# Kernel optimization log

Measured on AMD Instinct MI355X. Metric: run time of the kernel, lower is better.

Reference implementation:

```python
import jax, jax.numpy as jnp
import numpy as np

B, S, D, H, DFF, NL, VOCAB, SRC = 16, 128, 768, 12, 3072, 6, 32000, 256


def _pe_table():
    pos = np.arange(S)[:, None].astype(np.float32)
    div = np.exp(np.arange(0, D, 2).astype(np.float32) * (-np.log(10000.0) / D))
    pe = np.zeros((S, D), np.float32)
    pe[:, 0::2] = np.sin(pos * div)
    pe[:, 1::2] = np.cos(pos * div)
    return jnp.asarray(pe)


def _ln(x, a, b, eps=1e-6):
    m = jnp.mean(x, axis=-1, keepdims=True)
    v = jnp.mean((x - m) ** 2, axis=-1, keepdims=True)
    return a * (x - m) / jnp.sqrt(v + eps) + b


def _mha(q_in, k_in, v_in, mask, Wq, bq, Wk, bk, Wv, bv, Wo, bo):
    Bq, Sq, Dm = q_in.shape
    Sk = k_in.shape[1]
    dk = Dm // H
    q = (q_in @ Wq + bq).reshape(Bq, Sq, H, dk).transpose(0, 2, 1, 3)
    k = (k_in @ Wk + bk).reshape(Bq, Sk, H, dk).transpose(0, 2, 1, 3)
    v = (v_in @ Wv + bv).reshape(Bq, Sk, H, dk).transpose(0, 2, 1, 3)
    s = jnp.einsum('bhqd,bhkd->bhqk', q, k) / jnp.sqrt(jnp.float32(dk))
    if mask is not None:
        s = jnp.where(mask == 0, jnp.float32(-1e9), s)
    a = jax.nn.softmax(s, axis=-1)
    o = jnp.einsum('bhqk,bhkd->bhqd', a, v).transpose(0, 2, 1, 3).reshape(Bq, Sq, Dm)
    return o @ Wo + bo


def _combined_mask(trg):
    # Vectorized, faithful replica of create_combined_mask (incl. its cumulative
    # cross-batch zeroing: for j in 0..B-2, if padding_start[j]!=0 zero rows
    # >= padding_start[j] of ALL batches b >= j).
    b, s = trg.shape
    is_pad = (trg == 0)
    haspad = jnp.any(is_pad, axis=1)
    start = jnp.where(haspad, jnp.argmax(is_pad, axis=1), 0)  # first pad idx, 0 if none
    c = jnp.where(start == 0, s + 1, start)                   # sentinel = never cut
    cmin = jax.lax.cummin(c)
    r = cmin[jnp.minimum(jnp.arange(b), b - 2)]               # effective cutoff per batch
    look = jnp.tril(jnp.ones((s, s), jnp.float32))
    keep = (jnp.arange(s)[None, :] < r[:, None]).astype(jnp.float32)  # (B,S) rows kept
    return (look[None] * keep[:, :, None])[:, None]           # (B,1,S,S)


def setup_inputs():
    key = jax.random.key(0)
    ks = jax.random.split(key, 16)
    tok = jax.random.randint(ks[0], (B, S), 1, VOCAB)
    lens = jax.random.randint(ks[1], (B,), S // 2, S + 1)
    trg = jnp.where(jnp.arange(S)[None, :] < lens[:, None], tok, 0).astype(jnp.int32)
    e_outputs = jax.random.normal(ks[2], (B, SRC, D), dtype=jnp.float32)
    src_mask = jax.random.randint(ks[3], (B, 1, 1, SRC), 0, 2).at[..., 0].set(1).astype(jnp.int32)
    w = lambda k, shape: (jax.random.normal(k, shape) * 0.02).astype(jnp.float32)
    emb = (jax.random.normal(ks[4], (VOCAB, D)) * 0.1).astype(jnp.float32).at[0].set(0.0)
    return {
        'trg': trg, 'e_outputs': e_outputs, 'src_mask': src_mask,
        'emb': emb,
        'y_param': jax.random.normal(ks[5], (S, D), dtype=jnp.float32),
        'pe_alpha': jnp.float32(1.0),
        'Wq': w(ks[6], (NL, 3, D, D)), 'Wk': w(ks[7], (NL, 3, D, D)),
        'Wv': w(ks[8], (NL, 3, D, D)), 'Wo': w(ks[9], (NL, 3, D, D)),
        'bq': jnp.zeros((NL, 3, D)), 'bk': jnp.zeros((NL, 3, D)),
        'bv': jnp.zeros((NL, 3, D)), 'bo': jnp.zeros((NL, 3, D)),
        'W1': w(ks[10], (NL, D, DFF)), 'b1': jnp.zeros((NL, DFF)),
        'W2': w(ks[11], (NL, DFF, D)), 'b2': jnp.zeros((NL, D)),
        'ln_a': jnp.ones((NL, 5, D)), 'ln_b': jnp.zeros((NL, 5, D)),
        'final_a': jnp.ones((D,)), 'final_b': jnp.zeros((D,)),
    }


def reference(trg, e_outputs, src_mask, emb, y_param, pe_alpha, Wq, Wk, Wv, Wo,
              bq, bk, bv, bo, W1, b1, W2, b2, ln_a, ln_b, final_a, final_b):
    x = emb[trg] + pe_alpha * _pe_table()            # embedding + scaled PE
    y = jnp.broadcast_to(y_param, (trg.shape[0],) + y_param.shape)
    trg_mask = _combined_mask(trg)
    for i in range(Wq.shape[0]):
        x2 = _ln(x, ln_a[i, 0], ln_b[i, 0])
        x = x + _mha(x2, x2, x2, trg_mask, Wq[i, 0], bq[i, 0], Wk[i, 0], bk[i, 0], Wv[i, 0], bv[i, 0], Wo[i, 0], bo[i, 0])
        y2 = _ln(y, ln_a[i, 1], ln_b[i, 1])
        y = y + _mha(y2, e_outputs, e_outputs, src_mask, Wq[i, 1], bq[i, 1], Wk[i, 1], bk[i, 1], Wv[i, 1], bv[i, 1], Wo[i, 1], bo[i, 1])
        x2 = _ln(x, ln_a[i, 2], ln_b[i, 2])
        y3 = _ln(y, ln_a[i, 3], ln_b[i, 3])
        x = x + _mha(x2, y3, y3, None, Wq[i, 2], bq[i, 2], Wk[i, 2], bk[i, 2], Wv[i, 2], bv[i, 2], Wo[i, 2], bo[i, 2])
        x2 = _ln(x, ln_a[i, 4], ln_b[i, 4])
        x = x + jnp.maximum(x2 @ W1[i] + b1[i], 0.0) @ W2[i] + b2[i]
    return _ln(x, final_a, final_b)
```

## Files before the change

kernel.cpp:

```cpp
#include <hip/hip_runtime.h>
#include <math.h>

#define BB 16
#define SS 128
#define DD 768
#define HH 12
#define DKK 64
#define DFFF 3072
#define NLL 6
#define SRCC 256

typedef short bf16x8 __attribute__((ext_vector_type(8)));
typedef float f32x4 __attribute__((ext_vector_type(4)));
typedef unsigned short us8 __attribute__((ext_vector_type(8)));
typedef unsigned short us4 __attribute__((ext_vector_type(4)));

__device__ __forceinline__ unsigned short f2bf(float f) {
  unsigned int u = __builtin_bit_cast(unsigned int, f);
  u = (u + 0x7fff + ((u >> 16) & 1)) >> 16;
  return (unsigned short)u;
}

#define GLOADLDS16(gp, lp)                                              \
  __builtin_amdgcn_global_load_lds(                                     \
      (const __attribute__((address_space(1))) void*)(gp),              \
      (__attribute__((address_space(3))) void*)(lp), 16, 0, 0)

__global__ void embjoint_k(const int* __restrict__ trg, const float* __restrict__ emb,
                           const float* __restrict__ alpha,
                           const float* __restrict__ yp,
                           float* __restrict__ x, float* __restrict__ y) {
  int idx = blockIdx.x * blockDim.x + threadIdx.x;
  int c = idx % (DD / 4);
  int r = idx / (DD / 4);
  if (r >= BB * SS) return;
  int s = r % SS;
  if (blockIdx.y == 0) {
    float al = alpha[0];
    float4 e = *(const float4*)(emb + (size_t)trg[r] * DD + c * 4);
    float coef = -logf(10000.0f) / (float)DD;
    float div0 = expf((float)(4 * c) * coef);
    float div1 = expf((float)(4 * c + 2) * coef);
    float s0, c0, s1, c1;
    sincosf((float)s * div0, &s0, &c0);
    sincosf((float)s * div1, &s1, &c1);
    float4 o;
    o.x = e.x + al * s0; o.y = e.y + al * c0;
    o.z = e.z + al * s1; o.w = e.w + al * c1;
    *(float4*)(x + (size_t)r * DD + c * 4) = o;
  } else {
    *(float4*)(y + (size_t)r * DD + c * 4) = *(const float4*)(yp + (size_t)s * DD + c * 4);
  }
}

__global__ void mb_k(const int* __restrict__ trg, int* __restrict__ rbuf,
                     const float* __restrict__ bq, const float* __restrict__ bk,
                     const float* __restrict__ bv, float* __restrict__ bqkv1,
                     float* __restrict__ bkv2, float* __restrict__ bqkv3) {
  int t = threadIdx.x;
  if (blockIdx.x == 0) {
    __shared__ int first[BB];
    if (t < BB) first[t] = 0x7fffffff;
    __syncthreads();
    int b = t >> 4, p0 = (t & 15) * 8;
    int loc = 0x7fffffff;
#pragma unroll
    for (int i = 0; i < 8; i++) {
      if (trg[b * SS + p0 + i] == 0) { loc = p0 + i; break; }
    }
    atomicMin(&first[b], loc);
    __syncthreads();
    if (t == 0) {
      int cmin = 0x7fffffff;
      int cm[BB];
      for (int bb = 0; bb < BB; bb++) {
        int start = (first[bb] == 0x7fffffff) ? 0 : first[bb];
        int c = (start == 0) ? (SS + 1) : start;
        cmin = min(cmin, c);
        cm[bb] = cmin;
      }
      for (int bb = 0; bb < BB; bb++) rbuf[bb] = cm[min(bb, BB - 2)];
    }
    return;
  }
  int i = (blockIdx.x - 1) * 256 + t;
  if (i >= NLL * 6144) return;
  int l = i / 6144, j = i - l * 6144;
  if (j < 2304) {
    int s = j / 768, c = j - s * 768;
    const float* src = (s == 0) ? bq : (s == 1 ? bk : bv);
    bqkv1[l * 2304 + j] = src[(l * 3 + 0) * 768 + c];
  } else if (j < 3840) {
    int jj = j - 2304;
    int s = jj / 768, c = jj - s * 768;
    bkv2[l * 1536 + jj] = ((s == 0) ? bk : bv)[(l * 3 + 1) * 768 + c];
  } else {
    int jj = j - 3840;
    int s = jj / 768, c = jj - s * 768;
    const float* src = (s == 0) ? bq : (s == 1 ? bk : bv);
    bqkv3[l * 2304 + jj] = src[(l * 3 + 2) * 768 + c];
  }
}

__global__ __launch_bounds__(256) void ln_k(const float* __restrict__ x,
                                            const float* __restrict__ ga,
                                            const float* __restrict__ gb,
                                            float* __restrict__ out) {
  __shared__ float sm[8];
  int row = blockIdx.x;
  int t = threadIdx.x;
  const float* xr = x + (size_t)row * DD;
  float v0 = xr[t], v1 = xr[t + 256], v2 = xr[t + 512];
  float s = v0 + v1 + v2;
#pragma unroll
  for (int o = 32; o > 0; o >>= 1) s += __shfl_down(s, o);
  if ((t & 63) == 0) sm[t >> 6] = s;
  __syncthreads();
  float mean = (sm[0] + sm[1] + sm[2] + sm[3]) * (1.0f / (float)DD);
  float d0 = v0 - mean, d1 = v1 - mean, d2 = v2 - mean;
  float q = d0 * d0 + d1 * d1 + d2 * d2;
#pragma unroll
  for (int o = 32; o > 0; o >>= 1) q += __shfl_down(q, o);
  if ((t & 63) == 0) sm[4 + (t >> 6)] = q;
  __syncthreads();
  float var = (sm[4] + sm[5] + sm[6] + sm[7]) * (1.0f / (float)DD);
  float inv = 1.0f / sqrtf(var + 1e-6f);
  float* orow = out + (size_t)row * DD;
  orow[t]       = ga[t] * d0 * inv + gb[t];
  orow[t + 256] = ga[t + 256] * d1 * inv + gb[t + 256];
  orow[t + 512] = ga[t + 512] * d2 * inv + gb[t + 512];
}

__device__ __forceinline__ void lnb_body(const float* __restrict__ xr,
                                         const float* __restrict__ ga,
                                         const float* __restrict__ gb,
                                         unsigned short* __restrict__ orow,
                                         float* sm, int t) {
  float v0 = xr[t], v1 = xr[t + 256], v2 = xr[t + 512];
  float s = v0 + v1 + v2;
#pragma unroll
  for (int o = 32; o > 0; o >>= 1) s += __shfl_down(s, o);
  if ((t & 63) == 0) sm[t >> 6] = s;
  __syncthreads();
  float mean = (sm[0] + sm[1] + sm[2] + sm[3]) * (1.0f / (float)DD);
  float d0 = v0 - mean, d1 = v1 - mean, d2 = v2 - mean;
  float q = d0 * d0 + d1 * d1 + d2 * d2;
#pragma unroll
  for (int o = 32; o > 0; o >>= 1) q += __shfl_down(q, o);
  if ((t & 63) == 0) sm[4 + (t >> 6)] = q;
  __syncthreads();
  float var = (sm[4] + sm[5] + sm[6] + sm[7]) * (1.0f / (float)DD);
  float inv = 1.0f / sqrtf(var + 1e-6f);
  orow[t]       = f2bf(ga[t] * d0 * inv + gb[t]);
  orow[t + 256] = f2bf(ga[t + 256] * d1 * inv + gb[t + 256]);
  orow[t + 512] = f2bf(ga[t + 512] * d2 * inv + gb[t + 512]);
}

__global__ __launch_bounds__(256) void lnb_k(const float* __restrict__ x,
                                             const float* __restrict__ ga,
                                             const float* __restrict__ gb,
                                             unsigned short* __restrict__ out) {
  __shared__ float sm[8];
  int row = blockIdx.x;
  lnb_body(x + (size_t)row * DD, ga, gb, out + (size_t)row * DD, sm, threadIdx.x);
}

__global__ __launch_bounds__(256) void lnb2_k(const float* __restrict__ x,
                                              const float* __restrict__ y,
                                              const float* __restrict__ gax,
                                              const float* __restrict__ gbx,
                                              const float* __restrict__ gay,
                                              const float* __restrict__ gby,
                                              unsigned short* __restrict__ ox,
                                              unsigned short* __restrict__ oy) {
  __shared__ float sm[8];
  int row = blockIdx.x;
  if (row < BB * SS)
    lnb_body(x + (size_t)row * DD, gax, gbx, ox + (size_t)row * DD, sm, threadIdx.x);
  else {
    row -= BB * SS;
    lnb_body(y + (size_t)row * DD, gay, gby, oy + (size_t)row * DD, sm, threadIdx.x);
  }
}

__device__ __forceinline__ void tr_tile(const float* __restrict__ s,
                                        unsigned short* __restrict__ d,
                                        int K, int N, int k0, int n0,
                                        float (*tl)[69], int t) {
#pragma unroll
  for (int i = 0; i < 8; i++) {
    int c = t + i * 256;
    int row = c >> 4, c4 = (c & 15) * 4;
    float4 v = *(const float4*)(s + (size_t)(k0 + row) * N + n0 + c4);
    tl[row][c4 + 0] = v.x; tl[row][c4 + 1] = v.y;
    tl[row][c4 + 2] = v.z; tl[row][c4 + 3] = v.w;
  }
  __syncthreads();
#pragma unroll
  for (int i = 0; i < 4; i++) {
    int c = t + i * 256;
    int n = c >> 4, kc = c & 15;
    us8 o;
#pragma unroll
    for (int j = 0; j < 8; j++) o[j] = f2bf(tl[kc * 8 + j][n]);
    *(us8*)(d + (size_t)(n0 + n) * K + k0 + kc * 8) = o;
  }
}

__global__ __launch_bounds__(256) void wtx_k(
    const float* __restrict__ Wq, const float* __restrict__ Wk,
    const float* __restrict__ Wv, const float* __restrict__ Wo,
    const float* __restrict__ W1, const float* __restrict__ W2,
    const float* __restrict__ e_out,
    unsigned short* __restrict__ wqkv1A, unsigned short* __restrict__ wq2A,
    unsigned short* __restrict__ wkv2A, unsigned short* __restrict__ wqkv3A,
    unsigned short* __restrict__ wotA,
    unsigned short* __restrict__ w1tA, unsigned short* __restrict__ w2tA,
    unsigned short* __restrict__ eob) {
  __shared__ float tl[128][69];
  const size_t M1 = (size_t)DD * DD;
  int bid = blockIdx.x;
  int t = threadIdx.x;
  if (bid < 5184) {
    int mat = bid / 72, rem = bid % 72;
    int kt = rem / 12, nt = rem % 12;
    int l = mat / 12, m = mat % 12;
    size_t s3 = (size_t)l * 3 * M1;
    const float* s;
    unsigned short* d;
    switch (m) {
      case 0:  s = Wq + s3;          d = wqkv1A + l * 3 * M1;          break;
      case 1:  s = Wk + s3;          d = wqkv1A + l * 3 * M1 + M1;     break;
      case 2:  s = Wv + s3;          d = wqkv1A + l * 3 * M1 + 2 * M1; break;
      case 3:  s = Wq + s3 + M1;     d = wq2A + l * M1;                break;
      case 4:  s = Wk + s3 + M1;     d = wkv2A + l * 2 * M1;           break;
      case 5:  s = Wv + s3 + M1;     d = wkv2A + l * 2 * M1 + M1;      break;
      case 6:  s = Wq + s3 + 2 * M1; d = wqkv3A + l * 3 * M1;          break;
      case 7:  s = Wk + s3 + 2 * M1; d = wqkv3A + l * 3 * M1 + M1;     break;
      case 8:  s = Wv + s3 + 2 * M1; d = wqkv3A + l * 3 * M1 + 2 * M1; break;
      case 9:  s = Wo + s3;          d = wotA + l * 3 * M1;            break;
      case 10: s = Wo + s3 + M1;     d = wotA + l * 3 * M1 + M1;       break;
      default: s = Wo + s3 + 2 * M1; d = wotA + l * 3 * M1 + 2 * M1;   break;
    }
    tr_tile(s, d, DD, DD, kt * 128, nt * 64, tl, t);
  } else if (bid < 6912) {
    int idx = bid - 5184;
    int l = idx / 288, rem = idx % 288;
    int kt = rem / 48, nt = rem % 48;
    tr_tile(W1 + (size_t)l * DD * DFFF, w1tA + (size_t)l * DD * DFFF,
            DD, DFFF, kt * 128, nt * 64, tl, t);
  } else if (bid < 8640) {
    int idx = bid - 6912;
    int l = idx / 288, rem = idx % 288;
    int kt = rem / 12, nt = rem % 12;
    tr_tile(W2 + (size_t)l * DFFF * DD, w2tA + (size_t)l * DFFF * DD,
            DFFF, DD, kt * 128, nt * 64, tl, t);
  } else {
    size_t base = (size_t)(bid - 8640) * 2048 + (size_t)t * 8;
    float4 a = *(const float4*)(e_out + base);
    float4 b = *(const float4*)(e_out + base + 4);
    us8 o;
    o[0] = f2bf(a.x); o[1] = f2bf(a.y); o[2] = f2bf(a.z); o[3] = f2bf(a.w);
    o[4] = f2bf(b.x); o[5] = f2bf(b.y); o[6] = f2bf(b.z); o[7] = f2bf(b.w);
    *(us8*)(eob + base) = o;
  }
}

#define GEMM_BODY(BM, A, Bt, m0, n0)                                          \
  constexpr int FM = (BM) / 32;                                               \
  constexpr int HB = (BM) / 2;                                                \
  int wave = t >> 6, lane = t & 63;                                           \
  int wm = wave >> 1, wn = wave & 1;                                          \
  f32x4 acc[FM][2] = {};                                                      \
  int aRow = t >> 2, aC8 = (t & 3) * 8;                                       \
  const unsigned short* Ab = (A) + (size_t)(m0)*768 + aC8;                    \
  const unsigned short* Bb = (Bt) + (size_t)(n0)*768 + aC8;                   \
  int aOff0 = (wm * HB + (lane & 15)) * 32 + (lane >> 4) * 8;                 \
  int bOff0 = (wn * 32 + (lane & 15)) * 32 + (lane >> 4) * 8;                 \
  for (int k0 = 0; k0 < 768; k0 += 32) {                                      \
    _Pragma("unroll")                                                         \
    for (int h = 0; h < (BM) / 64; h++)                                       \
      GLOADLDS16(Ab + (size_t)(h * 64 + aRow) * 768 + k0,                     \
                 As + h * 2048 + wave * 512);                                 \
    GLOADLDS16(Bb + (size_t)aRow * 768 + k0, Bs + wave * 512);                \
    __syncthreads();                                                          \
    bf16x8 aF[FM], bF[2];                                                     \
    _Pragma("unroll")                                                         \
    for (int fm = 0; fm < FM; fm++)                                           \
      aF[fm] = *(const bf16x8*)(As + aOff0 + fm * 16 * 32);                   \
    _Pragma("unroll")                                                         \
    for (int fn = 0; fn < 2; fn++)                                            \
      bF[fn] = *(const bf16x8*)(Bs + bOff0 + fn * 16 * 32);                   \
    _Pragma("unroll")                                                         \
    for (int fm = 0; fm < FM; fm++)                                           \
      _Pragma("unroll")                                                       \
      for (int fn = 0; fn < 2; fn++)                                          \
        acc[fm][fn] = __builtin_amdgcn_mfma_f32_16x16x32_bf16(                \
            aF[fm], bF[fn], acc[fm][fn], 0, 0, 0);                            \
    __syncthreads();                                                          \
  }                                                                           \
  int lcol = lane & 15, lrow4 = (lane >> 4) * 4;

__device__ __forceinline__ void hm_store(unsigned short* hd, int sh, int vt,
                                         int rowb, int colr, const f32x4& a,
                                         float bv) {
  int hh = colr >> 6, dd = colr & 63;
  int bb = rowb >> sh, ssb = rowb & ((1 << sh) - 1);
  if (vt) {
    size_t idx = (((size_t)bb * HH + hh) * 64 + dd) * (size_t)(1 << sh) + ssb;
    us4 pk;
#pragma unroll
    for (int r = 0; r < 4; r++) pk[r] = f2bf(a[r] + bv);
    *(us4*)(hd + idx) = pk;
  } else {
    size_t base = ((((size_t)bb * HH + hh) << sh) + ssb) * 64 + dd;
#pragma unroll
    for (int r = 0; r < 4; r++) hd[base + (size_t)r * 64] = f2bf(a[r] + bv);
  }
}

template <int BM>
__global__ __launch_bounds__(256) void mgemm_k(
    const unsigned short* __restrict__ A0, const unsigned short* __restrict__ A1,
    const unsigned short* __restrict__ Bt, const float* __restrict__ bias,
    const float* __restrict__ res, void* __restrict__ C,
    unsigned short* __restrict__ hd0, unsigned short* __restrict__ hd1,
    unsigned short* __restrict__ hd2,
    int sh0, int sh1, int sh2, int M, int N, int K, int flags, int vtbits) {
  constexpr int FM = BM / 32;
  constexpr int HB = BM / 2;
  __shared__ unsigned short As[BM * 32];
  __shared__ unsigned short Bs[64 * 32];
  int t = threadIdx.x;
  int wave = t >> 6, lane = t & 63;
  int m0 = blockIdx.y * BM, n0 = blockIdx.x * 64;
  int seg = n0 / 768;
  const unsigned short* A = (seg == 0) ? A0 : A1;
  int wm = wave >> 1, wn = wave & 1;
  f32x4 acc[FM][2] = {};
  int aRow = t >> 2, aC8 = (t & 3) * 8;
  const unsigned short* Ab = A + (size_t)m0 * K + aC8;
  const unsigned short* Bb = Bt + (size_t)n0 * K + aC8;
  int aOff0 = (wm * HB + (lane & 15)) * 32 + (lane >> 4) * 8;
  int bOff0 = (wn * 32 + (lane & 15)) * 32 + (lane >> 4) * 8;
  for (int k0 = 0; k0 < K; k0 += 32) {
#pragma unroll
    for (int h = 0; h < BM / 64; h++)
      GLOADLDS16(Ab + (size_t)(h * 64 + aRow) * K + k0, As + h * 2048 + wave * 512);
    GLOADLDS16(Bb + (size_t)aRow * K + k0, Bs + wave * 512);
    __syncthreads();
    bf16x8 aF[FM], bF[2];
#pragma unroll
    for (int fm = 0; fm < FM; fm++)
      aF[fm] = *(const bf16x8*)(As + aOff0 + fm * 16 * 32);
#pragma unroll
    for (int fn = 0; fn < 2; fn++)
      bF[fn] = *(const bf16x8*)(Bs + bOff0 + fn * 16 * 32);
#pragma unroll
    for (int fm = 0; fm < FM; fm++)
#pragma unroll
      for (int fn = 0; fn < 2; fn++)
        acc[fm][fn] = __builtin_amdgcn_mfma_f32_16x16x32_bf16(aF[fm], bF[fn], acc[fm][fn], 0, 0, 0);
    __syncthreads();
  }
  int lcol = lane & 15, lrow4 = (lane >> 4) * 4;
  bool hm = (flags & 4) != 0;
  unsigned short* hd = nullptr;
  int sh = 0, segBase = seg * 768, vtseg = 0;
  if (hm) {
    hd = (seg == 0) ? hd0 : (seg == 1 ? hd1 : hd2);
    sh = (seg == 0) ? sh0 : (seg == 1 ? sh1 : sh2);
    vtseg = (vtbits >> seg) & 1;
  }
#pragma unroll
  for (int fm = 0; fm < FM; fm++) {
#pragma unroll
    for (int fn = 0; fn < 2; fn++) {
      int col = n0 + wn * 32 + fn * 16 + lcol;
      float bv = bias[col];
      int rowb = m0 + wm * HB + fm * 16 + lrow4;
      if (hm) {
        hm_store(hd, sh, vtseg, rowb, col - segBase, acc[fm][fn], bv);
      } else {
#pragma unroll
        for (int r = 0; r < 4; r++) {
          int row = rowb + r;
          float v = acc[fm][fn][r] + bv;
          size_t idx = (size_t)row * N + col;
          if (res) v += res[idx];
          if (flags & 1) v = fmaxf(v, 0.f);
          if (flags & 2) ((unsigned short*)C)[idx] = f2bf(v);
          else ((float*)C)[idx] = v;
        }
      }
    }
  }
}

__global__ __launch_bounds__(256) void kv2all_k(
    const unsigned short* __restrict__ eob, const unsigned short* __restrict__ wkv2A,
    const float* __restrict__ bkv2,
    unsigned short* __restrict__ khb2A, unsigned short* __restrict__ vthb2A) {
  __shared__ unsigned short As[128 * 32];
  __shared__ unsigned short Bs[64 * 32];
  const size_t M1 = (size_t)DD * DD;
  const size_t KVS = (size_t)BB * HH * SRCC * DKK;
  int t = threadIdx.x;
  int l = blockIdx.z;
  int m0 = blockIdx.y * 128, n0 = blockIdx.x * 64;
  const unsigned short* Bt = wkv2A + (size_t)l * 2 * M1;
  const float* bias = bkv2 + l * 1536;
  GEMM_BODY(128, eob, Bt, m0, n0)
  int seg = n0 / 768;
  unsigned short* hd = (seg == 0) ? khb2A + (size_t)l * KVS : vthb2A + (size_t)l * KVS;
  int vt = seg;
  int segBase = seg * 768;
#pragma unroll
  for (int fm = 0; fm < FM; fm++) {
#pragma unroll
    for (int fn = 0; fn < 2; fn++) {
      int col = n0 + wn * 32 + fn * 16 + lcol;
      int rowb = m0 + wm * HB + fm * 16 + lrow4;
      hm_store(hd, 8, vt, rowb, col - segBase, acc[fm][fn], bias[col]);
    }
  }
}

__global__ __launch_bounds__(256) void qkvq_k(
    const unsigned short* __restrict__ x2b, const unsigned short* __restrict__ y1b,
    const unsigned short* __restrict__ Bqkv, const unsigned short* __restrict__ Bq2,
    const float* __restrict__ bias1, const float* __restrict__ bias2,
    unsigned short* __restrict__ qhb, unsigned short* __restrict__ khb,
    unsigned short* __restrict__ vthb, unsigned short* __restrict__ qhb2) {
  __shared__ unsigned short As[128 * 32];
  __shared__ unsigned short Bs[64 * 32];
  int t = threadIdx.x;
  int bid = blockIdx.x;
  bool j1 = bid >= 576;
  int bx, by;
  const unsigned short *A, *Bt;
  const float* bias;
  if (!j1) { bx = bid % 36; by = bid / 36; A = x2b; Bt = Bqkv; bias = bias1; }
  else { int b2 = bid - 576; bx = b2 % 12; by = b2 / 12; A = y1b; Bt = Bq2; bias = bias2; }
  int m0 = by * 128, n0 = bx * 64;
  GEMM_BODY(128, A, Bt, m0, n0)
  int seg = j1 ? 0 : (n0 / 768);
  unsigned short* hd = j1 ? qhb2 : (seg == 0 ? qhb : (seg == 1 ? khb : vthb));
  int vt = (!j1 && seg == 2) ? 1 : 0;
  int segBase = seg * 768;
#pragma unroll
  for (int fm = 0; fm < FM; fm++) {
#pragma unroll
    for (int fn = 0; fn < 2; fn++) {
      int col = n0 + wn * 32 + fn * 16 + lcol;
      int rowb = m0 + wm * HB + fm * 16 + lrow4;
      hm_store(hd, 7, vt, rowb, col - segBase, acc[fm][fn], bias[col]);
    }
  }
}

__global__ __launch_bounds__(256) void wob_k(
    const unsigned short* __restrict__ ctx1b, const unsigned short* __restrict__ ctx2b,
    const unsigned short* __restrict__ Bt0, const unsigned short* __restrict__ Bt1,
    const float* __restrict__ bo0, const float* __restrict__ bo1,
    float* __restrict__ x, float* __restrict__ y) {
  __shared__ unsigned short As[64 * 32];
  __shared__ unsigned short Bs[64 * 32];
  int t = threadIdx.x;
  int bid = blockIdx.x;
  bool j1 = bid >= 384;
  int b2 = j1 ? bid - 384 : bid;
  int bx = b2 % 12, by = b2 / 12;
  const unsigned short* A = j1 ? ctx2b : ctx1b;
  const unsigned short* Bt = j1 ? Bt1 : Bt0;
  const float* bias = j1 ? bo1 : bo0;
  float* C = j1 ? y : x;
  int m0 = by * 64, n0 = bx * 64;
  GEMM_BODY(64, A, Bt, m0, n0)
#pragma unroll
  for (int fm = 0; fm < FM; fm++) {
#pragma unroll
    for (int fn = 0; fn < 2; fn++) {
      int col = n0 + wn * 32 + fn * 16 + lcol;
      float bv = bias[col];
      int rowb = m0 + wm * HB + fm * 16 + lrow4;
#pragma unroll
      for (int r = 0; r < 4; r++) {
        size_t idx = (size_t)(rowb + r) * DD + col;
        C[idx] += acc[fm][fn][r] + bv;
      }
    }
  }
}

template <int SK>
__global__ __launch_bounds__(256) void attn3_k(const unsigned short* __restrict__ qh,
                                               const unsigned short* __restrict__ kh,
                                               const unsigned short* __restrict__ vth,
                                               unsigned short* __restrict__ ctxb, int mode,
                                               const int* __restrict__ rbuf,
                                               const int* __restrict__ smask) {
  constexpr int NPH = SK / 128;
  constexpr int NF = SK / 16;
  __shared__ unsigned short kvb[128 * 72];
  __shared__ unsigned short pbuf[64 * (SK + 8)];
  int qhalf = blockIdx.x, h = blockIdx.y, b = blockIdx.z;
  int t = threadIdx.x;
  int wave = t >> 6, lane = t & 63;
  int l15 = lane & 15, lhi = lane >> 4;
  int qrow0 = qhalf * 64 + wave * 16;
  size_t bh = (size_t)b * HH + h;
  bf16x8 aQ[2];
#pragma unroll
  for (int ks = 0; ks < 2; ks++)
    aQ[ks] = *(const bf16x8*)(qh + (bh * SS + qrow0 + l15) * 64 + ks * 32 + lhi * 8);
  f32x4 accS[NF] = {};
  const unsigned short* kbase = kh + bh * SK * 64;
  for (int ph = 0; ph < NPH; ph++) {
    if (ph) __syncthreads();
    {
      int c0 = t * 4;
#pragma unroll
      for (int i = 0; i < 4; i++) {
        int c = c0 + i, row = c >> 3, co = (c & 7) * 8;
        *(us8*)&kvb[row * 72 + co] = *(const us8*)(kbase + (size_t)(ph * 128 + row) * 64 + co);
      }
    }
    __syncthreads();
#pragma unroll
    for (int kf = 0; kf < 8; kf++) {
      int gf = ph * 8 + kf;
#pragma unroll
      for (int ks = 0; ks < 2; ks++) {
        bf16x8 bK = *(const bf16x8*)(&kvb[(kf * 16 + l15) * 72 + ks * 32 + lhi * 8]);
        accS[gf] = __builtin_amdgcn_mfma_f32_16x16x32_bf16(aQ[ks], bK, accS[gf], 0, 0, 0);
      }
    }
  }
  int rcut = (mode == 0) ? rbuf[b] : 0;
#pragma unroll
  for (int r = 0; r < 4; r++) {
    int qg = qrow0 + lhi * 4 + r;
    float mx = -3.4e38f;
#pragma unroll
    for (int gf = 0; gf < NF; gf++) {
      int k = gf * 16 + l15;
      float s = accS[gf][r] * 0.125f;
      bool keep = true;
      if (mode == 0) keep = (k <= qg) && (qg < rcut);
      else if (mode == 1) keep = (smask[b * SRCC + k] != 0);
      s = keep ? s : -1e9f;
      accS[gf][r] = s;
      mx = fmaxf(mx, s);
    }
#pragma unroll
    for (int o = 1; o < 16; o <<= 1) mx = fmaxf(mx, __shfl_xor(mx, o));
    float sum = 0.f;
#pragma unroll
    for (int gf = 0; gf < NF; gf++) {
      float e = expf(accS[gf][r] - mx);
      accS[gf][r] = e;
      sum += e;
    }
#pragma unroll
    for (int o = 1; o < 16; o <<= 1) sum += __shfl_xor(sum, o);
    float rinv = 1.0f / sum;
#pragma unroll
    for (int gf = 0; gf < NF; gf++) accS[gf][r] *= rinv;
  }
#pragma unroll
  for (int gf = 0; gf < NF; gf++) {
#pragma unroll
    for (int r = 0; r < 4; r++) {
      int ql = wave * 16 + lhi * 4 + r;
      pbuf[ql * (SK + 8) + gf * 16 + l15] = f2bf(accS[gf][r]);
    }
  }
  __syncthreads();
  f32x4 accO[4] = {};
  const unsigned short* vbase = vth + bh * 64 * SK;
  for (int ph = 0; ph < NPH; ph++) {
    if (ph) __syncthreads();
    {
      int c0 = t * 4;
#pragma unroll
      for (int i = 0; i < 4; i++) {
        int c = c0 + i, row = c >> 4, co = (c & 15) * 8;
        *(us8*)&kvb[row * 136 + co] = *(const us8*)(vbase + (size_t)row * SK + ph * 128 + co);
      }
    }
    __syncthreads();
#pragma unroll
    for (int ks = 0; ks < 4; ks++) {
      bf16x8 aP = *(const bf16x8*)(&pbuf[(wave * 16 + l15) * (SK + 8) + ph * 128 + ks * 32 + lhi * 8]);
#pragma unroll
      for (int nf = 0; nf < 4; nf++) {
        bf16x8 bV = *(const bf16x8*)(&kvb[(nf * 16 + l15) * 136 + ks * 32 + lhi * 8]);
        accO[nf] = __builtin_amdgcn_mfma_f32_16x16x32_bf16(aP, bV, accO[nf], 0, 0, 0);
      }
    }
  }
#pragma unroll
  for (int nf = 0; nf < 4; nf++) {
#pragma unroll
    for (int r = 0; r < 4; r++) {
      int qg = qrow0 + lhi * 4 + r;
      ctxb[((size_t)b * SS + qg) * DD + h * 64 + nf * 16 + l15] = f2bf(accO[nf][r]);
    }
  }
}

extern "C" void kernel_launch(void* const* d_in, const int* in_sizes, int n_in,
                              void* d_out, int out_size, void* d_ws, size_t ws_size,
                              hipStream_t stream) {
  const int*   trg   = (const int*)d_in[0];
  const float* e_out = (const float*)d_in[1];
  const int*   smask = (const int*)d_in[2];
  const float* emb   = (const float*)d_in[3];
  const float* ypar  = (const float*)d_in[4];
  const float* alpha = (const float*)d_in[5];
  const float* Wq = (const float*)d_in[6];
  const float* Wk = (const float*)d_in[7];
  const float* Wv = (const float*)d_in[8];
  const float* Wo = (const float*)d_in[9];
  const float* bq = (const float*)d_in[10];
  const float* bk = (const float*)d_in[11];
  const float* bv = (const float*)d_in[12];
  const float* bo = (const float*)d_in[13];
  const float* W1 = (const float*)d_in[14];
  const float* b1 = (const float*)d_in[15];
  const float* W2 = (const float*)d_in[16];
  const float* b2 = (const float*)d_in[17];
  const float* lna = (const float*)d_in[18];
  const float* lnbp = (const float*)d_in[19];
  const float* fa = (const float*)d_in[20];
  const float* fb = (const float*)d_in[21];
  float* out = (float*)d_out;

  float* ws = (float*)d_ws;
  size_t off = 0;
  auto alloc = [&](size_t n) { float* p = ws + off; off += n; return p; };
  const size_t M1 = (size_t)DD * DD;
  const size_t KVS = (size_t)BB * HH * SRCC * DKK;
  int* rbuf  = (int*)alloc(64);
  float* x   = alloc((size_t)BB * SS * DD);
  float* y   = alloc((size_t)BB * SS * DD);
  float* bqkv1 = alloc((size_t)NLL * 2304);
  float* bkv2  = alloc((size_t)NLL * 1536);
  float* bqkv3 = alloc((size_t)NLL * 2304);
  unsigned short* qhb   = (unsigned short*)alloc((size_t)BB * HH * SS * DKK / 2);
  unsigned short* qhb2  = (unsigned short*)alloc((size_t)BB * HH * SS * DKK / 2);
  unsigned short* khb   = (unsigned short*)alloc((size_t)BB * HH * SS * DKK / 2);
  unsigned short* vthb  = (unsigned short*)alloc((size_t)BB * HH * SS * DKK / 2);
  unsigned short* khb2A  = (unsigned short*)alloc((size_t)NLL * KVS / 2);
  unsigned short* vthb2A = (unsigned short*)alloc((size_t)NLL * KVS / 2);
  unsigned short* x2b   = (unsigned short*)alloc((size_t)BB * SS * DD / 2);
  unsigned short* y3b   = (unsigned short*)alloc((size_t)BB * SS * DD / 2);
  unsigned short* ctx1b = (unsigned short*)alloc((size_t)BB * SS * DD / 2);
  unsigned short* ctx2b = (unsigned short*)alloc((size_t)BB * SS * DD / 2);
  unsigned short* midb  = (unsigned short*)alloc((size_t)BB * SS * DFFF / 2);
  unsigned short* eob   = (unsigned short*)alloc((size_t)BB * SRCC * DD / 2);
  unsigned short* wqkv1A = (unsigned short*)alloc((size_t)NLL * 3 * M1 / 2);
  unsigned short* wq2A   = (unsigned short*)alloc((size_t)NLL * M1 / 2);
  unsigned short* wkv2A  = (unsigned short*)alloc((size_t)NLL * 2 * M1 / 2);
  unsigned short* wqkv3A = (unsigned short*)alloc((size_t)NLL * 3 * M1 / 2);
  unsigned short* wotA   = (unsigned short*)alloc((size_t)NLL * 3 * M1 / 2);
  unsigned short* w1tA   = (unsigned short*)alloc((size_t)NLL * DD * DFFF / 2);
  unsigned short* w2tA   = (unsigned short*)alloc((size_t)NLL * DFFF * DD / 2);
  if (ws_size < off * sizeof(float)) return;

  embjoint_k<<<dim3((BB * SS * (DD / 4) + 255) / 256, 2), 256, 0, stream>>>(
      trg, emb, alpha, ypar, x, y);
  mb_k<<<1 + (NLL * 6144 + 255) / 256, 256, 0, stream>>>(trg, rbuf, bq, bk, bv,
                                                         bqkv1, bkv2, bqkv3);
  wtx_k<<<10176, 256, 0, stream>>>(Wq, Wk, Wv, Wo, W1, W2, e_out,
                                   wqkv1A, wq2A, wkv2A, wqkv3A, wotA, w1tA, w2tA, eob);
  kv2all_k<<<dim3(24, 32, NLL), 256, 0, stream>>>(eob, wkv2A, bkv2, khb2A, vthb2A);

  auto MG128 = [&](const unsigned short* A0, const unsigned short* A1, int M, int K,
                   const unsigned short* Bt, int N, const float* bias, const float* res,
                   void* C, unsigned short* h0, unsigned short* h1, unsigned short* h2,
                   int s0, int s1, int s2, int flags, int vtb) {
    mgemm_k<128><<<dim3(N / 64, M / 128), 256, 0, stream>>>(A0, A1, Bt, bias, res, C,
                                                            h0, h1, h2, s0, s1, s2, M, N, K, flags, vtb);
  };
  auto MG64 = [&](const unsigned short* A0, int M, int K,
                  const unsigned short* Bt, int N, const float* bias, const float* res,
                  void* C, unsigned short* h0, int s0, int flags, int vtb) {
    mgemm_k<64><<<dim3(N / 64, M / 64), 256, 0, stream>>>(A0, A0, Bt, bias, res, C,
                                                          h0, nullptr, nullptr, s0, 0, 0, M, N, K, flags, vtb);
  };
  const dim3 agrid(SS / 64, HH, BB);

  for (int l = 0; l < NLL; l++) {
    const float* lA = lna + (size_t)l * 5 * DD;
    const float* lB = lnbp + (size_t)l * 5 * DD;
    lnb2_k<<<2 * BB * SS, 256, 0, stream>>>(x, y, lA, lB, lA + DD, lB + DD, x2b, y3b);
    qkvq_k<<<768, 256, 0, stream>>>(x2b, y3b, wqkv1A + l * 3 * M1, wq2A + l * M1,
                                    bqkv1 + l * 2304, bq + ((size_t)l * 3 + 1) * DD,
                                    qhb, khb, vthb, qhb2);
    attn3_k<SS><<<agrid, 256, 0, stream>>>(qhb, khb, vthb, ctx1b, 0, rbuf, nullptr);
    attn3_k<SRCC><<<agrid, 256, 0, stream>>>(qhb2, khb2A + l * KVS, vthb2A + l * KVS,
                                             ctx2b, 1, nullptr, smask);
    wob_k<<<768, 256, 0, stream>>>(ctx1b, ctx2b, wotA + l * 3 * M1, wotA + l * 3 * M1 + M1,
                                   bo + (size_t)l * 3 * DD, bo + ((size_t)l * 3 + 1) * DD, x, y);
    lnb2_k<<<2 * BB * SS, 256, 0, stream>>>(x, y, lA + 2 * DD, lB + 2 * DD,
                                            lA + 3 * DD, lB + 3 * DD, x2b, y3b);
    MG128(x2b, y3b, BB * SS, DD, wqkv3A + l * 3 * M1, 2304, bqkv3 + l * 2304, nullptr,
          nullptr, qhb, khb, vthb, 7, 7, 7, 4, 0b100);
    attn3_k<SS><<<agrid, 256, 0, stream>>>(qhb, khb, vthb, ctx1b, 2, nullptr, nullptr);
    MG64(ctx1b, BB * SS, DD, wotA + l * 3 * M1 + 2 * M1, DD, bo + ((size_t)l * 3 + 2) * DD,
         x, x, nullptr, 0, 0, 0);
    lnb_k<<<BB * SS, 256, 0, stream>>>(x, lA + 4 * DD, lB + 4 * DD, x2b);
    MG128(x2b, x2b, BB * SS, DD, w1tA + (size_t)l * DD * DFFF, DFFF, b1 + (size_t)l * DFFF,
          nullptr, midb, nullptr, nullptr, nullptr, 0, 0, 0, 3, 0);
    MG64(midb, BB * SS, DFFF, w2tA + (size_t)l * DFFF * DD, DD, b2 + (size_t)l * DD, x, x,
         nullptr, 0, 0, 0);
  }
  ln_k<<<BB * SS, 256, 0, stream>>>(x, fa, fb, out);
}
```

Measured before the change: 1.529 ms.

## Merge self and cross attention launches; use 128x128 tiles for cross-KV GEMM

```diff
diff --git a/kernel.cpp b/kernel.cpp
--- a/kernel.cpp
+++ b/kernel.cpp
@@ -402,25 +402,58 @@
     const float* __restrict__ bkv2,
     unsigned short* __restrict__ khb2A, unsigned short* __restrict__ vthb2A) {
   __shared__ unsigned short As[128 * 32];
-  __shared__ unsigned short Bs[64 * 32];
+  __shared__ unsigned short Bs[128 * 32];
   const size_t M1 = (size_t)DD * DD;
   const size_t KVS = (size_t)BB * HH * SRCC * DKK;
   int t = threadIdx.x;
-  int l = blockIdx.z;
-  int m0 = blockIdx.y * 128, n0 = blockIdx.x * 64;
+  int flat = blockIdx.x;
+  int nf = (flat & 7) * 288 + (flat >> 3);
+  int bx = nf % 12;
+  int rem = nf / 12;
+  int by = rem & 31;
+  int l = rem >> 5;
+  int m0 = by * 128, n0 = bx * 128;
   const unsigned short* Bt = wkv2A + (size_t)l * 2 * M1;
   const float* bias = bkv2 + l * 1536;
-  GEMM_BODY(128, eob, Bt, m0, n0)
+  int wave = t >> 6, lane = t & 63;
+  int wm = wave >> 1, wn = wave & 1;
+  f32x4 acc[4][4] = {};
+  int aRow = t >> 2, aC8 = (t & 3) * 8;
+  const unsigned short* Ab = eob + (size_t)m0 * 768 + aC8;
+  const unsigned short* Bb = Bt + (size_t)n0 * 768 + aC8;
+  int l15 = lane & 15, lhi = lane >> 4;
+  int aOff0 = (wm * 64 + l15) * 32 + lhi * 8;
+  int bOff0 = (wn * 64 + l15) * 32 + lhi * 8;
+  for (int k0 = 0; k0 < 768; k0 += 32) {
+    GLOADLDS16(Ab + (size_t)aRow * 768 + k0, As + wave * 512);
+    GLOADLDS16(Ab + (size_t)(64 + aRow) * 768 + k0, As + 2048 + wave * 512);
+    GLOADLDS16(Bb + (size_t)aRow * 768 + k0, Bs + wave * 512);
+    GLOADLDS16(Bb + (size_t)(64 + aRow) * 768 + k0, Bs + 2048 + wave * 512);
+    __syncthreads();
+    bf16x8 aF[4], bF[4];
+#pragma unroll
+    for (int fm = 0; fm < 4; fm++)
+      aF[fm] = *(const bf16x8*)(As + aOff0 + fm * 16 * 32);
+#pragma unroll
+    for (int fn = 0; fn < 4; fn++)
+      bF[fn] = *(const bf16x8*)(Bs + bOff0 + fn * 16 * 32);
+#pragma unroll
+    for (int fm = 0; fm < 4; fm++)
+#pragma unroll
+      for (int fn = 0; fn < 4; fn++)
+        acc[fm][fn] = __builtin_amdgcn_mfma_f32_16x16x32_bf16(aF[fm], bF[fn], acc[fm][fn], 0, 0, 0);
+    __syncthreads();
+  }
   int seg = n0 / 768;
   unsigned short* hd = (seg == 0) ? khb2A + (size_t)l * KVS : vthb2A + (size_t)l * KVS;
   int vt = seg;
   int segBase = seg * 768;
 #pragma unroll
-  for (int fm = 0; fm < FM; fm++) {
-#pragma unroll
-    for (int fn = 0; fn < 2; fn++) {
-      int col = n0 + wn * 32 + fn * 16 + lcol;
-      int rowb = m0 + wm * HB + fm * 16 + lrow4;
+  for (int fm = 0; fm < 4; fm++) {
+#pragma unroll
+    for (int fn = 0; fn < 4; fn++) {
+      int col = n0 + wn * 64 + fn * 16 + l15;
+      int rowb = m0 + wm * 64 + fm * 16 + lhi * 4;
       hm_store(hd, 8, vt, rowb, col - segBase, acc[fm][fn], bias[col]);
     }
   }
@@ -494,17 +527,14 @@
 }
 
 template <int SK>
-__global__ __launch_bounds__(256) void attn3_k(const unsigned short* __restrict__ qh,
-                                               const unsigned short* __restrict__ kh,
-                                               const unsigned short* __restrict__ vth,
-                                               unsigned short* __restrict__ ctxb, int mode,
-                                               const int* __restrict__ rbuf,
-                                               const int* __restrict__ smask) {
+__device__ __forceinline__ void attn_body(
+    const unsigned short* __restrict__ qh, const unsigned short* __restrict__ kh,
+    const unsigned short* __restrict__ vth, unsigned short* __restrict__ ctxb,
+    int mode, const int* __restrict__ rbuf, const int* __restrict__ smask,
+    unsigned short* __restrict__ kvb, unsigned short* __restrict__ pbuf,
+    int qhalf, int h, int b) {
   constexpr int NPH = SK / 128;
   constexpr int NF = SK / 16;
-  __shared__ unsigned short kvb[128 * 72];
-  __shared__ unsigned short pbuf[64 * (SK + 8)];
-  int qhalf = blockIdx.x, h = blockIdx.y, b = blockIdx.z;
   int t = threadIdx.x;
   int wave = t >> 6, lane = t & 63;
   int l15 = lane & 15, lhi = lane >> 4;
@@ -607,6 +637,41 @@
       int qg = qrow0 + lhi * 4 + r;
       ctxb[((size_t)b * SS + qg) * DD + h * 64 + nf * 16 + l15] = f2bf(accO[nf][r]);
     }
+  }
+}
+
+template <int SK>
+__global__ __launch_bounds__(256) void attn3_k(const unsigned short* __restrict__ qh,
+                                               const unsigned short* __restrict__ kh,
+                                               const unsigned short* __restrict__ vth,
+                                               unsigned short* __restrict__ ctxb, int mode,
+                                               const int* __restrict__ rbuf,
+                                               const int* __restrict__ smask) {
+  __shared__ unsigned short kvb[128 * 72];
+  __shared__ unsigned short pbuf[64 * (SK + 8)];
+  attn_body<SK>(qh, kh, vth, ctxb, mode, rbuf, smask, kvb, pbuf,
+                blockIdx.x, blockIdx.y, blockIdx.z);
+}
+
+__global__ __launch_bounds__(256) void attnboth_k(
+    const unsigned short* __restrict__ qh1, const unsigned short* __restrict__ kh1,
+    const unsigned short* __restrict__ vth1,
+    const unsigned short* __restrict__ qh2, const unsigned short* __restrict__ kh2,
+    const unsigned short* __restrict__ vth2,
+    unsigned short* __restrict__ ctx1b, unsigned short* __restrict__ ctx2b,
+    const int* __restrict__ rbuf, const int* __restrict__ smask) {
+  __shared__ unsigned short kvb[128 * 72];
+  __shared__ unsigned short pbuf[64 * (SRCC + 8)];
+  int bid = blockIdx.x;
+  if (bid < 384) {
+    int qhalf = bid & 1, rest = bid >> 1;
+    int h = rest % HH, b = rest / HH;
+    attn_body<SRCC>(qh2, kh2, vth2, ctx2b, 1, nullptr, smask, kvb, pbuf, qhalf, h, b);
+  } else {
+    int b2 = bid - 384;
+    int qhalf = b2 & 1, rest = b2 >> 1;
+    int h = rest % HH, b = rest / HH;
+    attn_body<SS>(qh1, kh1, vth1, ctx1b, 0, rbuf, nullptr, kvb, pbuf, qhalf, h, b);
   }
 }
 
@@ -675,7 +740,7 @@
                                                          bqkv1, bkv2, bqkv3);
   wtx_k<<<10176, 256, 0, stream>>>(Wq, Wk, Wv, Wo, W1, W2, e_out,
                                    wqkv1A, wq2A, wkv2A, wqkv3A, wotA, w1tA, w2tA, eob);
-  kv2all_k<<<dim3(24, 32, NLL), 256, 0, stream>>>(eob, wkv2A, bkv2, khb2A, vthb2A);
+  kv2all_k<<<2304, 256, 0, stream>>>(eob, wkv2A, bkv2, khb2A, vthb2A);
 
   auto MG128 = [&](const unsigned short* A0, const unsigned short* A1, int M, int K,
                    const unsigned short* Bt, int N, const float* bias, const float* res,
@@ -699,9 +764,9 @@
     qkvq_k<<<768, 256, 0, stream>>>(x2b, y3b, wqkv1A + l * 3 * M1, wq2A + l * M1,
                                     bqkv1 + l * 2304, bq + ((size_t)l * 3 + 1) * DD,
                                     qhb, khb, vthb, qhb2);
-    attn3_k<SS><<<agrid, 256, 0, stream>>>(qhb, khb, vthb, ctx1b, 0, rbuf, nullptr);
-    attn3_k<SRCC><<<agrid, 256, 0, stream>>>(qhb2, khb2A + l * KVS, vthb2A + l * KVS,
-                                             ctx2b, 1, nullptr, smask);
+    attnboth_k<<<768, 256, 0, stream>>>(qhb, khb, vthb,
+                                        qhb2, khb2A + l * KVS, vthb2A + l * KVS,
+                                        ctx1b, ctx2b, rbuf, smask);
     wob_k<<<768, 256, 0, stream>>>(ctx1b, ctx2b, wotA + l * 3 * M1, wotA + l * 3 * M1 + M1,
                                    bo + (size_t)l * 3 * DD, bo + ((size_t)l * 3 + 1) * DD, x, y);
     lnb2_k<<<2 * BB * SS, 256, 0, stream>>>(x, y, lA + 2 * DD, lB + 2 * DD,
```

Result: faster. 1.435 ms (-6.2%).
